# Kernel tuning notes

Measured on AMD Instinct MI355X. Metric: run time of the kernel, lower is better.

## Reference

```python
import jax, jax.numpy as jnp
import numpy as np

DIM, H, D, B, L = 1024, 8, 64, 1, 256


def silu(v):
    return v * jax.nn.sigmoid(v)


def setup_inputs() -> dict:
    key = jax.random.key(0)
    ks = jax.random.split(key, 12)
    n = lambda i, shape, scale=1.0: jax.random.normal(ks[i], shape, dtype=jnp.float32) * scale
    return {
        "x": n(0, (B, L, DIM)),
        "hidden_real": n(1, (B, H, D)),
        "hidden_imag": n(2, (B, H, D)),
        "w_in1": n(3, (DIM, DIM), 1.0 / np.sqrt(DIM)),
        "b_in1": jnp.zeros((DIM,), jnp.float32),
        "w_in2": n(4, (DIM, H * D * 4), 1.0 / np.sqrt(DIM)),
        "b_in2": jnp.zeros((H * D * 4,), jnp.float32),
        "w_out1": n(5, (H * D * 2, DIM), 1.0 / np.sqrt(H * D * 2)),
        "b_out1": jnp.zeros((DIM,), jnp.float32),
        "w_out2": n(6, (DIM, DIM), 1.0 / np.sqrt(DIM)),
        "b_out2": jnp.zeros((DIM,), jnp.float32),
        "mat_v_real": n(7, (H, D, D)),
        "mat_v_imag": n(8, (H, D, D)),
    }


def reference(x, hidden_real, hidden_imag, w_in1, b_in1, w_in2, b_in2,
              w_out1, b_out1, w_out2, b_out2, mat_v_real, mat_v_imag):
    batch, slen, _ = x.shape
    t = silu(x @ w_in1 + b_in1)
    t = t @ w_in2 + b_in2                       # (B, L, 4*H*D)
    z = t.reshape(batch, slen, H, D, 2, 2)      # [..., {x,a}, {re,im}]
    xc = jax.lax.complex(z[..., 0, 0], z[..., 0, 1])   # (B, L, H, D) complex
    ac = jax.lax.complex(z[..., 1, 0], z[..., 1, 1])

    # normalize a: unit phase * sigmoid(log(|a|^2)) magnitude
    mag2 = ac.real * ac.real + ac.imag * ac.imag
    ac = ac * (jax.lax.rsqrt(mag2) * jax.nn.sigmoid(jnp.log(mag2)))

    a_ln = jnp.log(ac)                          # (B, L, H, D) complex
    al = jnp.transpose(a_ln, (0, 2, 3, 1))      # (B, H, D, L)

    # triu-broadcast + cumsum along cols == the FFT conv-with-ones in the original
    idx = jnp.arange(slen)
    triu = idx[:, None] <= idx[None, :]          # row i, col j: keep j >= i
    tri = jnp.where(triu, al[..., None, :], 0.0)  # (B, H, D, L, L)
    cum = jnp.cumsum(tri, axis=-1)               # cum[i, k] = sum_{j=i..k} a_ln[j]
    keep = (idx[:, None] - 1) <= idx[None, :]    # triu(diagonal=-1)
    c = jnp.where(keep, jnp.exp(cum), 0.0)       # c[i,k] = prod_{j=i..k} a[j]; c[i,i-1]=1

    V = jax.lax.complex(mat_v_real, mat_v_imag)  # (H, D, D)
    Vinv = jnp.linalg.inv(V)
    hidden = jax.lax.complex(hidden_real, hidden_imag)  # (B, H, D)

    x_roll = jnp.concatenate([hidden.astype(xc.dtype)[:, None], xc[:, :-1]], axis=1)
    u = jnp.einsum('hno,blho->blhn', Vinv, x_roll)       # V^{-1} applied per head
    h = jnp.einsum('bholm,blho->bmho', c, u)             # banded product-scan
    h = h.at[:, -1].add(jnp.einsum('hno,bho->bhn', Vinv, xc[:, -1]))
    h = jnp.einsum('hno,blho->blhn', V, h)               # back to V-basis

    hidden_next = h[:, -1]                                # (B, H, D) complex
    hr = jnp.stack([h.real, h.imag], axis=-1).reshape(batch, slen, H * D * 2)
    y = silu(hr @ w_out1 + b_out1)
    y = y @ w_out2 + b_out2
    return y, hidden_next
```

## Files before the change

### kernel.cpp

```cpp
#include <hip/hip_runtime.h>
#include <math.h>

#define DIMN 1024
#define NH 8
#define ND 64
#define LSEQ 256
#define HD 512

typedef __attribute__((ext_vector_type(8))) short short8;
typedef __attribute__((ext_vector_type(4))) float f32x4;

__device__ __forceinline__ float2 cmul(float2 a, float2 b){
    return make_float2(a.x*b.x - a.y*b.y, a.x*b.y + a.y*b.x);
}
__device__ __forceinline__ ushort f2bf(float f){
    union { float f; unsigned u; } v; v.f = f;
    unsigned r = v.u + 0x7FFF + ((v.u >> 16) & 1);
    return (ushort)(r >> 16);
}

#define ISTR 65

__device__ __forceinline__ void inv_gj_blocked(const float* __restrict__ Vr,
        const float* __restrict__ Vi, float2* __restrict__ Vinv,
        int h, int tid, float2* Mx){
    for (int idx = tid; idx < 4096; idx += 512){
        int i = idx >> 6, j = idx & 63;
        Mx[i*ISTR + j] = make_float2(Vr[h*4096 + idx], Vi[h*4096 + idx]);
    }
    __syncthreads();
    const int w = tid >> 6, l = tid & 63;
    const int rbase = w*8;
    for (int kb = 0; kb < 8; ++kb){
        const int k0 = kb*8;
        if (w == 0){
            float2 pr[8];
            #pragma unroll
            for (int m = 0; m < 8; ++m) pr[m] = Mx[l*ISTR + k0 + m];
            #pragma unroll
            for (int k = 0; k < 8; ++k){
                const int gk = k0 + k;
                float2 d; d.x = __shfl(pr[k].x, gk); d.y = __shfl(pr[k].y, gk);
                float im = 1.f/(d.x*d.x + d.y*d.y);
                float2 p = make_float2(d.x*im, -d.y*im);
                float2 spr[8];
                #pragma unroll
                for (int m = 0; m < 8; ++m){
                    float2 t; t.x = __shfl(pr[m].x, gk); t.y = __shfl(pr[m].y, gk);
                    spr[m] = (m == k) ? p : cmul(t, p);
                }
                float2 f = pr[k];
                if (l == gk){
                    #pragma unroll
                    for (int m = 0; m < 8; ++m) pr[m] = spr[m];
                } else {
                    #pragma unroll
                    for (int m = 0; m < 8; ++m){
                        float2 u = cmul(f, spr[m]);
                        if (m == k){ pr[m].x = -u.x;  pr[m].y = -u.y;  }
                        else       { pr[m].x -= u.x;  pr[m].y -= u.y;  }
                    }
                }
            }
            #pragma unroll
            for (int m = 0; m < 8; ++m) Mx[l*ISTR + k0 + m] = pr[m];
        }
        __syncthreads();
        float2 br[8];
        #pragma unroll
        for (int m = 0; m < 8; ++m) br[m] = Mx[(k0+m)*ISTR + l];
        __syncthreads();
        if (((unsigned)(l - k0)) >= 8u){
            #pragma unroll
            for (int rr = 0; rr < 8; ++rr){
                const int r = rbase + rr;
                float2 acc;
                if (((unsigned)(r - k0)) < 8u){ acc.x = 0.f; acc.y = 0.f; }
                else acc = Mx[r*ISTR + l];
                #pragma unroll
                for (int m = 0; m < 8; ++m){
                    float2 Pv = Mx[r*ISTR + k0 + m];
                    acc.x += Pv.x*br[m].x - Pv.y*br[m].y;
                    acc.y += Pv.x*br[m].y + Pv.y*br[m].x;
                }
                Mx[r*ISTR + l] = acc;
            }
        }
        __syncthreads();
    }
    for (int idx = tid; idx < 4096; idx += 512){
        int i = idx >> 6, j = idx & 63;
        Vinv[h*4096 + idx] = Mx[i*ISTR + j];
    }
}

__device__ __forceinline__ void w3eff_tile(const float* __restrict__ Vr,
        const float* __restrict__ Vi, const float* __restrict__ w3,
        ushort* __restrict__ W3bt, int t, int tid, float* lds){
    const int n0 = (t & 31)*32;
    const int c0 = (t >> 5)*32;
    const int h  = c0 >> 7;
    const int og0 = (c0 & 127) >> 1;
    float* Vbr = lds;
    float* Vbi = lds + 1024;
    float* Wb  = lds + 2048;
    for (int q = tid; q < 1024; q += 512){
        int dd = q >> 4, oo = q & 15;
        Vbr[q] = Vr[(h*64+dd)*64 + og0 + oo];
        Vbi[q] = Vi[(h*64+dd)*64 + og0 + oo];
    }
    for (int q = tid; q < 4096; q += 512){
        int row = q >> 5, nn = q & 31;
        Wb[q] = w3[(h*128 + row)*1024 + n0 + nn];
    }
    __syncthreads();
    const int nn = tid & 31, oo = tid >> 5;
    float ar = 0.f, ai = 0.f;
    #pragma unroll 8
    for (int dd = 0; dd < 64; ++dd){
        float vr = Vbr[dd*16 + oo], vi = Vbi[dd*16 + oo];
        float w0 = Wb[(dd*2)*32 + nn], w1v = Wb[(dd*2+1)*32 + nn];
        ar += vr*w0 + vi*w1v;
        ai += -vi*w0 + vr*w1v;
    }
    W3bt[(n0+nn)*1024 + c0 + oo*2 + 0] = f2bf(ar);
    W3bt[(n0+nn)*1024 + c0 + oo*2 + 1] = f2bf(ai);
}

__global__ __launch_bounds__(512) void prep_kernel(
        const float* __restrict__ x,
        const float* __restrict__ w1, const float* __restrict__ w2,
        const float* __restrict__ w3, const float* __restrict__ w4,
        const float* __restrict__ Vr, const float* __restrict__ Vi,
        ushort* __restrict__ x_bf,
        ushort* __restrict__ w1t, ushort* __restrict__ w2t,
        ushort* __restrict__ W3bt, ushort* __restrict__ w4t,
        float2* __restrict__ Vinv){
    __shared__ float2 Mx[64*ISTR];
    const int b = blockIdx.x;
    const int tid = threadIdx.x;

    if (b < 8){
        inv_gj_blocked(Vr, Vi, Vinv, b, tid, Mx);
        return;
    }

    int widx = b - 8;
    if (widx < 128){
        int i = widx*512 + tid;
        float4 v = ((const float4*)x)[i];
        ushort4 u; u.x=f2bf(v.x); u.y=f2bf(v.y); u.z=f2bf(v.z); u.w=f2bf(v.w);
        ((ushort4*)x_bf)[i] = u;
        return;
    }
    widx -= 128;

    if (widx >= 2048){
        w3eff_tile(Vr, Vi, w3, W3bt, widx - 2048, tid, (float*)Mx);
        return;
    }

    const float* W; ushort* Wt; int K = 1024, N;
    if (widx < 512)            { W = w1; Wt = w1t; N = 1024; }
    else if (widx < 1536)      { W = w2; Wt = w2t; N = 2048; widx -= 512; }
    else                       { W = w4; Wt = w4t; N = 1024; widx -= 1536; }
    const int half = tid >> 8;
    const int t = widx*2 + half;
    const int tiles_n = N >> 5;
    const int n0 = (t % tiles_n) * 32, k0 = (t / tiles_n) * 32;
    float* tile = (float*)Mx + half*(32*33);
    const int tx = tid & 31, ty = (tid >> 5) & 7;
    #pragma unroll
    for (int i = 0; i < 4; ++i)
        tile[(ty + i*8)*33 + tx] = W[(k0 + ty + i*8)*N + n0 + tx];
    __syncthreads();
    #pragma unroll
    for (int i = 0; i < 4; ++i){
        int r = ty + i*8;
        Wt[(n0 + r)*K + k0 + tx] = f2bf(tile[tx*33 + r]);
    }
}

__global__ __launch_bounds__(512) void inv_kernel(const float* __restrict__ Vr,
                                                  const float* __restrict__ Vi,
                                                  float2* __restrict__ Vinv){
    __shared__ float2 Mx[64*ISTR];
    inv_gj_blocked(Vr, Vi, Vinv, blockIdx.x, threadIdx.x, Mx);
}

__global__ __launch_bounds__(256) void transpose_cvt(const float* __restrict__ W,
                 ushort* __restrict__ Wt, int K, int N){
    __shared__ float tile[32][33];
    const int n0 = blockIdx.x * 32, k0 = blockIdx.y * 32;
    const int tx = threadIdx.x & 31, ty = threadIdx.x >> 5;
    #pragma unroll
    for (int i = 0; i < 4; ++i)
        tile[ty + i*8][tx] = W[(k0 + ty + i*8)*N + n0 + tx];
    __syncthreads();
    #pragma unroll
    for (int i = 0; i < 4; ++i){
        int r = ty + i*8;
        Wt[(n0 + r)*K + k0 + tx] = f2bf(tile[tx][r]);
    }
}

__global__ __launch_bounds__(256) void cvt_bf16_kernel(const float* __restrict__ in,
                                 ushort* __restrict__ o, int n4){
    int i = blockIdx.x*256 + threadIdx.x;
    if (i < n4){
        float4 v = ((const float4*)in)[i];
        ushort4 u; u.x=f2bf(v.x); u.y=f2bf(v.y); u.z=f2bf(v.z); u.w=f2bf(v.w);
        ((ushort4*)o)[i] = u;
    }
}

#define BM 64
#define BN 64
#define BK 32
#define ASTR 40
template<int ACT>
__global__ __launch_bounds__(256) void gemm_bt(const ushort* __restrict__ A,
                 const ushort* __restrict__ Bt, const float* __restrict__ bias,
                 float* __restrict__ Cf, ushort* __restrict__ Cb,
                 float2* __restrict__ XCo, float2* __restrict__ Ao,
                 int M, int N, int K,
                 const float* __restrict__ tVr, const float* __restrict__ tVi,
                 const float2* __restrict__ S255, float* __restrict__ out_tail,
                 int tail_n){
    __shared__ ushort As[BM*ASTR];
    __shared__ ushort Bs[BN*ASTR];
    const int tid = threadIdx.x;
    const int bm = blockIdx.y * BM, bn = blockIdx.x * BN;
    const int wave = tid >> 6, l = tid & 63;
    const int wr = (wave >> 1) * 32, wc = (wave & 1) * 32;
    const int ml = l & 15, quad = l >> 4;

    if (ACT == 0 && out_tail != nullptr && blockIdx.x == 0 && blockIdx.y == 0){
        for (int hn = tid; hn < 512; hn += 256){
            int h = hn >> 6;
            float2 acc2 = make_float2(0.f, 0.f);
            #pragma unroll 8
            for (int o = 0; o < 64; ++o){
                float2 v = make_float2(tVr[hn*64+o], tVi[hn*64+o]);
                float2 p = cmul(v, S255[h*64+o]);
                acc2.x += p.x; acc2.y += p.y;
            }
            if (tail_n >= 1024){
                out_tail[hn]       = acc2.x;
                out_tail[512 + hn] = acc2.y;
            } else if (tail_n >= 512){
                out_tail[hn] = acc2.x;
            }
        }
    }

    f32x4 acc[2][2];
    #pragma unroll
    for (int i=0;i<2;++i)
        #pragma unroll
        for (int j=0;j<2;++j) acc[i][j] = (f32x4){0.f,0.f,0.f,0.f};
    const int c0r = tid >> 2;
    const int c0s = tid & 3;
    for (int k0 = 0; k0 < K; k0 += BK){
        uint4 av = *(const uint4*)&A [(bm + c0r)*K + k0 + c0s*8];
        uint4 bv = *(const uint4*)&Bt[(bn + c0r)*K + k0 + c0s*8];
        __syncthreads();
        *(uint4*)&As[c0r*ASTR + c0s*8] = av;
        *(uint4*)&Bs[c0r*ASTR + c0s*8] = bv;
        __syncthreads();
        short8 af[2], bfv[2];
        #pragma unroll
        for (int f=0; f<2; ++f){
            af[f]  = *(const short8*)&As[(wr + f*16 + ml)*ASTR + quad*8];
            bfv[f] = *(const short8*)&Bs[(wc + f*16 + ml)*ASTR + quad*8];
        }
        #pragma unroll
        for (int i=0;i<2;++i)
            #pragma unroll
            for (int j=0;j<2;++j)
                acc[i][j] = __builtin_amdgcn_mfma_f32_16x16x32_bf16(af[i], bfv[j], acc[i][j], 0,0,0);
    }
    #pragma unroll
    for (int i=0;i<2;++i){
        #pragma unroll
        for (int j=0;j<2;++j){
            const int gcol = bn + wc + j*16 + ml;
            const float bsv = bias[gcol];
            #pragma unroll
            for (int r=0;r<4;++r){
                const int grow = bm + wr + i*16 + quad*4 + r;
                float val = acc[i][j][r] + bsv;
                if (ACT == 2){
                    float v1 = __shfl_down(val, 1);
                    float v2 = __shfl_down(val, 2);
                    float v3 = __shfl_down(val, 3);
                    if ((l & 3) == 0){
                        int hd = gcol >> 2;
                        XCo[grow*HD + hd] = make_float2(val, v1);
                        float m2 = v2*v2 + v3*v3;
                        float s = sqrtf(m2)/(1.f + m2);
                        Ao[grow*HD + hd] = make_float2(v2*s, v3*s);
                    }
                } else if (ACT == 1){
                    val *= 1.f/(1.f + expf(-val));
                    Cb[grow*N + gcol] = f2bf(val);
                } else {
                    Cf[grow*N + gcol] = val;
                }
            }
        }
    }
}

__global__ __launch_bounds__(512) void upscan_kernel(const float2* __restrict__ Vinv,
        const float* __restrict__ hidr, const float* __restrict__ him,
        const float2* __restrict__ XC, const float2* __restrict__ Aseq,
        ushort* __restrict__ Sb, float2* __restrict__ S255){
    __shared__ float4 buf[2][2][LSEQ];
    __shared__ float2 vrow[2][64];
    __shared__ float2 inu[2];
    const int b = blockIdx.x;
    const int tid = threadIdx.x;
    const int g = tid >> 8, m = tid & 255;
    const int hn = b*2 + g;
    const int h = hn >> 6;
    if (m < 64) vrow[g][m] = Vinv[hn*64 + m];
    __syncthreads();
    float2 acc = make_float2(0.f, 0.f);
    const float2* xrow = &XC[m*HD + h*64];
    #pragma unroll 8
    for (int o=0;o<64;++o){
        float2 p = cmul(vrow[g][o], xrow[o]);
        acc.x += p.x; acc.y += p.y;
    }
    if (m == 0){
        float2 i0 = make_float2(0.f, 0.f);
        #pragma unroll 8
        for (int o=0;o<64;++o){
            float2 hv = make_float2(hidr[h*64+o], him[h*64+o]);
            float2 p = cmul(vrow[g][o], hv);
            i0.x += p.x; i0.y += p.y;
        }
        inu[g] = i0;
    }
    float2 a = Aseq[m*HD + hn];
    buf[0][g][m] = make_float4(a.x, a.y, acc.x, acc.y);
    __syncthreads();
    int pb = 0;
    #pragma unroll
    for (int d = 1; d < LSEQ; d <<= 1){
        float4 cur = buf[pb][g][m];
        float4 o2 = cur;
        if (m >= d){
            float4 prev = buf[pb][g][m-d];
            float2 cA = make_float2(cur.x, cur.y), cU = make_float2(cur.z, cur.w);
            float2 pA = make_float2(prev.x, prev.y), pU = make_float2(prev.z, prev.w);
            float2 nA = cmul(cA, pA);
            float2 nU = cmul(cA, pU);
            nU.x += cU.x; nU.y += cU.y;
            o2 = make_float4(nA.x, nA.y, nU.x, nU.y);
        }
        buf[pb^1][g][m] = o2;
        pb ^= 1;
        __syncthreads();
    }
    float4 t = buf[pb][g][m];
    float2 init = inu[g];
    float2 st = cmul(make_float2(t.x, t.y), init);
    st.x += t.z; st.y += t.w;
    Sb[m*DIMN + hn*2]   = f2bf(st.x);
    Sb[m*DIMN + hn*2+1] = f2bf(st.y);
    if (m == LSEQ-1) S255[hn] = st;
}

__global__ __launch_bounds__(256) void vmul_kernel(const float* __restrict__ Vr,
                            const float* __restrict__ Vi,
                            const float2* __restrict__ S, ushort* __restrict__ hrb,
                            float* __restrict__ out_tail, int tail_n){
    int g = blockIdx.x*256 + threadIdx.x;
    int m = g >> 9, hn = g & 511;
    int h = hn >> 6;
    const float* vr = &Vr[hn*64];
    const float* vi = &Vi[hn*64];
    const float2* srow = &S[m*HD + h*64];
    float2 acc = make_float2(0.f, 0.f);
    #pragma unroll 8
    for (int o=0;o<64;++o){
        float2 v = make_float2(vr[o], vi[o]);
        float2 p = cmul(v, srow[o]);
        acc.x += p.x; acc.y += p.y;
    }
    hrb[m*DIMN + hn*2]   = f2bf(acc.x);
    hrb[m*DIMN + hn*2+1] = f2bf(acc.y);
    if (m == LSEQ-1){
        if (tail_n >= 1024){
            out_tail[hn]       = acc.x;
            out_tail[512 + hn] = acc.y;
        } else if (tail_n >= 512){
            out_tail[hn] = acc.x;
        }
    }
}

__global__ __launch_bounds__(512) void upscan_f32_kernel(const float2* __restrict__ Vinv,
        const float* __restrict__ hidr, const float* __restrict__ him,
        const float2* __restrict__ XC, const float2* __restrict__ Aseq,
        float2* __restrict__ S){
    __shared__ float4 buf[2][2][LSEQ];
    __shared__ float2 vrow[2][64];
    __shared__ float2 inu[2];
    const int b = blockIdx.x;
    const int tid = threadIdx.x;
    const int g = tid >> 8, m = tid & 255;
    const int hn = b*2 + g;
    const int h = hn >> 6;
    if (m < 64) vrow[g][m] = Vinv[hn*64 + m];
    __syncthreads();
    float2 acc = make_float2(0.f, 0.f);
    const float2* xrow = &XC[m*HD + h*64];
    #pragma unroll 8
    for (int o=0;o<64;++o){
        float2 p = cmul(vrow[g][o], xrow[o]);
        acc.x += p.x; acc.y += p.y;
    }
    if (m == 0){
        float2 i0 = make_float2(0.f, 0.f);
        #pragma unroll 8
        for (int o=0;o<64;++o){
            float2 hv = make_float2(hidr[h*64+o], him[h*64+o]);
            float2 p = cmul(vrow[g][o], hv);
            i0.x += p.x; i0.y += p.y;
        }
        inu[g] = i0;
    }
    float2 a = Aseq[m*HD + hn];
    buf[0][g][m] = make_float4(a.x, a.y, acc.x, acc.y);
    __syncthreads();
    int pb = 0;
    #pragma unroll
    for (int d = 1; d < LSEQ; d <<= 1){
        float4 cur = buf[pb][g][m];
        float4 o2 = cur;
        if (m >= d){
            float4 prev = buf[pb][g][m-d];
            float2 cA = make_float2(cur.x, cur.y), cU = make_float2(cur.z, cur.w);
            float2 pA = make_float2(prev.x, prev.y), pU = make_float2(prev.z, prev.w);
            float2 nA = cmul(cA, pA);
            float2 nU = cmul(cA, pU);
            nU.x += cU.x; nU.y += cU.y;
            o2 = make_float4(nA.x, nA.y, nU.x, nU.y);
        }
        buf[pb^1][g][m] = o2;
        pb ^= 1;
        __syncthreads();
    }
    float4 t = buf[pb][g][m];
    float2 init = inu[g];
    float2 st = cmul(make_float2(t.x, t.y), init);
    st.x += t.z; st.y += t.w;
    S[m*HD + hn] = st;
}

extern "C" void kernel_launch(void* const* d_in, const int* in_sizes, int n_in,
                              void* d_out, int out_size, void* d_ws, size_t ws_size,
                              hipStream_t stream) {
    const float* x      = (const float*)d_in[0];
    const float* hidr   = (const float*)d_in[1];
    const float* hidi   = (const float*)d_in[2];
    const float* w_in1  = (const float*)d_in[3];
    const float* b_in1  = (const float*)d_in[4];
    const float* w_in2  = (const float*)d_in[5];
    const float* b_in2  = (const float*)d_in[6];
    const float* w_out1 = (const float*)d_in[7];
    const float* b_out1 = (const float*)d_in[8];
    const float* w_out2 = (const float*)d_in[9];
    const float* b_out2 = (const float*)d_in[10];
    const float* Vr     = (const float*)d_in[11];
    const float* Vi     = (const float*)d_in[12];
    float* out = (float*)d_out;
    const int tail_n = out_size - LSEQ*DIMN;
    char* ws = (char*)d_ws;

    if (ws_size >= 14946304u){
        float2* Vinv  = (float2*)(ws + 0);
        ushort* w1t   = (ushort*)(ws + 262144);
        ushort* w2t   = (ushort*)(ws + 2359296);
        ushort* W3bt  = (ushort*)(ws + 6553600);
        ushort* w4t   = (ushort*)(ws + 8650752);
        ushort* x_bf  = (ushort*)(ws + 10747904);
        ushort* t1_bf = (ushort*)(ws + 11272192);
        float2* XC    = (float2*)(ws + 11796480);
        float2* Aseq  = (float2*)(ws + 12845056);
        float2* S255  = (float2*)(ws + 13893632);
        ushort* y1_bf = x_bf;
        ushort* Sb    = t1_bf;

        prep_kernel<<<3208, 512, 0, stream>>>(x, w_in1, w_in2, w_out1, w_out2,
                                              Vr, Vi, x_bf, w1t, w2t, W3bt, w4t, Vinv);
        gemm_bt<1><<<dim3(16,4), 256, 0, stream>>>(x_bf, w1t, b_in1, nullptr, t1_bf,
                nullptr, nullptr, LSEQ, DIMN, DIMN, nullptr, nullptr, nullptr, nullptr, 0);
        gemm_bt<2><<<dim3(32,4), 256, 0, stream>>>(t1_bf, w2t, b_in2, nullptr, nullptr,
                XC, Aseq, LSEQ, 2048, DIMN, nullptr, nullptr, nullptr, nullptr, 0);
        upscan_kernel<<<256, 512, 0, stream>>>(Vinv, hidr, hidi, XC, Aseq, Sb, S255);
        gemm_bt<1><<<dim3(16,4), 256, 0, stream>>>(Sb, W3bt, b_out1, nullptr, y1_bf,
                nullptr, nullptr, LSEQ, DIMN, DIMN, nullptr, nullptr, nullptr, nullptr, 0);
        gemm_bt<0><<<dim3(16,4), 256, 0, stream>>>(y1_bf, w4t, b_out2, out, nullptr,
                nullptr, nullptr, LSEQ, DIMN, DIMN, Vr, Vi, S255, out + LSEQ*DIMN, tail_n);
    } else {
        float2* Vinv  = (float2*)(ws + 0);
        ushort* wt    = (ushort*)(ws + 262144);
        ushort* x_bf  = (ushort*)(ws + 4456448);
        ushort* t1_bf = (ushort*)(ws + 4980736);
        float2* XC    = (float2*)(ws + 5505024);
        float2* Aseq  = (float2*)(ws + 6553600);
        float2* S     = (float2*)(ws + 7602176);
        ushort* y1_bf = x_bf;
        ushort* hr_bf = t1_bf;

        inv_kernel<<<NH, 512, 0, stream>>>(Vr, Vi, Vinv);
        cvt_bf16_kernel<<<LSEQ*DIMN/4/256, 256, 0, stream>>>(x, x_bf, LSEQ*DIMN/4);
        transpose_cvt<<<dim3(32,32), 256, 0, stream>>>(w_in1, wt, DIMN, DIMN);
        gemm_bt<1><<<dim3(16,4), 256, 0, stream>>>(x_bf, wt, b_in1, nullptr, t1_bf,
                nullptr, nullptr, LSEQ, DIMN, DIMN, nullptr, nullptr, nullptr, nullptr, 0);
        transpose_cvt<<<dim3(64,32), 256, 0, stream>>>(w_in2, wt, DIMN, 2048);
        gemm_bt<2><<<dim3(32,4), 256, 0, stream>>>(t1_bf, wt, b_in2, nullptr, nullptr,
                XC, Aseq, LSEQ, 2048, DIMN, nullptr, nullptr, nullptr, nullptr, 0);
        upscan_f32_kernel<<<256, 512, 0, stream>>>(Vinv, hidr, hidi, XC, Aseq, S);
        vmul_kernel<<<LSEQ*HD/256, 256, 0, stream>>>(Vr, Vi, S, hr_bf, out + LSEQ*DIMN, tail_n);
        transpose_cvt<<<dim3(32,32), 256, 0, stream>>>(w_out1, wt, DIMN, DIMN);
        gemm_bt<1><<<dim3(16,4), 256, 0, stream>>>(hr_bf, wt, b_out1, nullptr, y1_bf,
                nullptr, nullptr, LSEQ, DIMN, DIMN, nullptr, nullptr, nullptr, nullptr, 0);
        transpose_cvt<<<dim3(32,32), 256, 0, stream>>>(w_out2, wt, DIMN, DIMN);
        gemm_bt<0><<<dim3(16,4), 256, 0, stream>>>(y1_bf, wt, b_out2, out, nullptr,
                nullptr, nullptr, LSEQ, DIMN, DIMN, nullptr, nullptr, nullptr, nullptr, 0);
    }
}
```

Before: 212.7 us.

## Fuse first GEMM into prep kernel reading fp32 x and w1 directly

The first GEMM (x @ w_in1 + bias, SiLU) now runs inside the prep kernel as 32 extra blocks, each computing two 64x64 tiles. These tiles load fp32 x and w1 directly and convert to bf16 in LDS. This removes the separate x conversion, the w1 transpose/convert pass and one kernel launch. The cost is that the GEMM runs alongside the other prep work with no software pipelining, and it does strided scalar loads of w1 that may be poorly coalesced.

```diff
diff --git a/kernel.cpp b/kernel.cpp
--- a/kernel.cpp
+++ b/kernel.cpp
@@ -20,6 +20,8 @@
 }
 
 #define ISTR 65
+#define ASTR 40
+#define BK 32
 
 __device__ __forceinline__ void inv_gj_blocked(const float* __restrict__ Vr,
         const float* __restrict__ Vi, float2* __restrict__ Vinv,
@@ -127,48 +129,102 @@
     W3bt[(n0+nn)*1024 + c0 + oo*2 + 1] = f2bf(ai);
 }
 
-__global__ __launch_bounds__(512) void prep_kernel(
+__device__ __forceinline__ void gemm1_direct_tile(const float* __restrict__ x,
+        const float* __restrict__ w1, const float* __restrict__ bias,
+        ushort* __restrict__ Cb, int tile, int tid8, ushort* lds){
+    ushort* As = lds;
+    ushort* Bs = lds + 64*ASTR;
+    const int bm = (tile & 3)*64, bn = (tile >> 2)*64;
+    const int wave = tid8 >> 6, l = tid8 & 63;
+    const int wr = (wave >> 1)*32, wc = (wave & 1)*32;
+    const int ml = l & 15, quad = l >> 4;
+    f32x4 acc[2][2];
+    #pragma unroll
+    for (int i=0;i<2;++i)
+        #pragma unroll
+        for (int j=0;j<2;++j) acc[i][j] = (f32x4){0.f,0.f,0.f,0.f};
+    const int c0r = tid8 >> 2, c0s = tid8 & 3;
+    const int bn_n = tid8 & 63, bk0 = (tid8 >> 6)*8;
+    for (int k0 = 0; k0 < DIMN; k0 += BK){
+        float4 a0 = *(const float4*)&x[(bm+c0r)*DIMN + k0 + c0s*8];
+        float4 a1 = *(const float4*)&x[(bm+c0r)*DIMN + k0 + c0s*8 + 4];
+        float bv[8];
+        #pragma unroll
+        for (int kk = 0; kk < 8; ++kk)
+            bv[kk] = w1[(k0 + bk0 + kk)*DIMN + bn + bn_n];
+        __syncthreads();
+        ushort4 u0; u0.x=f2bf(a0.x); u0.y=f2bf(a0.y); u0.z=f2bf(a0.z); u0.w=f2bf(a0.w);
+        ushort4 u1; u1.x=f2bf(a1.x); u1.y=f2bf(a1.y); u1.z=f2bf(a1.z); u1.w=f2bf(a1.w);
+        *(ushort4*)&As[c0r*ASTR + c0s*8]     = u0;
+        *(ushort4*)&As[c0r*ASTR + c0s*8 + 4] = u1;
+        #pragma unroll
+        for (int kk = 0; kk < 8; ++kk)
+            Bs[bn_n*ASTR + bk0 + kk] = f2bf(bv[kk]);
+        __syncthreads();
+        short8 af[2], bfv[2];
+        #pragma unroll
+        for (int f=0; f<2; ++f){
+            af[f]  = *(const short8*)&As[(wr + f*16 + ml)*ASTR + quad*8];
+            bfv[f] = *(const short8*)&Bs[(wc + f*16 + ml)*ASTR + quad*8];
+        }
+        #pragma unroll
+        for (int i=0;i<2;++i)
+            #pragma unroll
+            for (int j=0;j<2;++j)
+                acc[i][j] = __builtin_amdgcn_mfma_f32_16x16x32_bf16(af[i], bfv[j], acc[i][j], 0,0,0);
+    }
+    #pragma unroll
+    for (int i=0;i<2;++i){
+        #pragma unroll
+        for (int j=0;j<2;++j){
+            const int gcol = bn + wc + j*16 + ml;
+            const float bsv = bias[gcol];
+            #pragma unroll
+            for (int r=0;r<4;++r){
+                const int grow = bm + wr + i*16 + quad*4 + r;
+                float val = acc[i][j][r] + bsv;
+                val *= 1.f/(1.f + expf(-val));
+                Cb[grow*DIMN + gcol] = f2bf(val);
+            }
+        }
+    }
+}
+
+__global__ __launch_bounds__(512) void mix1_kernel(
         const float* __restrict__ x,
         const float* __restrict__ w1, const float* __restrict__ w2,
         const float* __restrict__ w3, const float* __restrict__ w4,
         const float* __restrict__ Vr, const float* __restrict__ Vi,
-        ushort* __restrict__ x_bf,
-        ushort* __restrict__ w1t, ushort* __restrict__ w2t,
-        ushort* __restrict__ W3bt, ushort* __restrict__ w4t,
-        float2* __restrict__ Vinv){
-    __shared__ float2 Mx[64*ISTR];
+        const float* __restrict__ b1,
+        ushort* __restrict__ t1_bf,
+        ushort* __restrict__ w2t, ushort* __restrict__ W3bt,
+        ushort* __restrict__ w4t, float2* __restrict__ Vinv){
+    __shared__ __align__(16) char lds_raw[33280];
     const int b = blockIdx.x;
     const int tid = threadIdx.x;
-
-    if (b < 8){
-        inv_gj_blocked(Vr, Vi, Vinv, b, tid, Mx);
+    const int half = tid >> 8;
+
+    if (b < 32){
+        gemm1_direct_tile(x, w1, b1, t1_bf, b*2 + half, tid & 255,
+                          (ushort*)lds_raw + half*(128*ASTR));
         return;
     }
-
-    int widx = b - 8;
-    if (widx < 128){
-        int i = widx*512 + tid;
-        float4 v = ((const float4*)x)[i];
-        ushort4 u; u.x=f2bf(v.x); u.y=f2bf(v.y); u.z=f2bf(v.z); u.w=f2bf(v.w);
-        ((ushort4*)x_bf)[i] = u;
+    if (b < 40){
+        inv_gj_blocked(Vr, Vi, Vinv, b - 32, tid, (float2*)lds_raw);
         return;
     }
-    widx -= 128;
-
-    if (widx >= 2048){
-        w3eff_tile(Vr, Vi, w3, W3bt, widx - 2048, tid, (float*)Mx);
+    int widx = b - 40;
+    if (widx >= 1536){
+        w3eff_tile(Vr, Vi, w3, W3bt, widx - 1536, tid, (float*)lds_raw);
         return;
     }
-
     const float* W; ushort* Wt; int K = 1024, N;
-    if (widx < 512)            { W = w1; Wt = w1t; N = 1024; }
-    else if (widx < 1536)      { W = w2; Wt = w2t; N = 2048; widx -= 512; }
-    else                       { W = w4; Wt = w4t; N = 1024; widx -= 1536; }
-    const int half = tid >> 8;
+    if (widx < 1024){ W = w2; Wt = w2t; N = 2048; }
+    else            { W = w4; Wt = w4t; N = 1024; widx -= 1024; }
     const int t = widx*2 + half;
     const int tiles_n = N >> 5;
     const int n0 = (t % tiles_n) * 32, k0 = (t / tiles_n) * 32;
-    float* tile = (float*)Mx + half*(32*33);
+    float* tile = (float*)lds_raw + half*(32*33);
     const int tx = tid & 31, ty = (tid >> 5) & 7;
     #pragma unroll
     for (int i = 0; i < 4; ++i)
@@ -216,8 +272,6 @@
 
 #define BM 64
 #define BN 64
-#define BK 32
-#define ASTR 40
 template<int ACT>
 __global__ __launch_bounds__(256) void gemm_bt(const ushort* __restrict__ A,
                  const ushort* __restrict__ Bt, const float* __restrict__ bias,
@@ -483,22 +537,18 @@
 
     if (ws_size >= 14946304u){
         float2* Vinv  = (float2*)(ws + 0);
-        ushort* w1t   = (ushort*)(ws + 262144);
         ushort* w2t   = (ushort*)(ws + 2359296);
         ushort* W3bt  = (ushort*)(ws + 6553600);
         ushort* w4t   = (ushort*)(ws + 8650752);
-        ushort* x_bf  = (ushort*)(ws + 10747904);
+        ushort* y1_bf = (ushort*)(ws + 10747904);
         ushort* t1_bf = (ushort*)(ws + 11272192);
         float2* XC    = (float2*)(ws + 11796480);
         float2* Aseq  = (float2*)(ws + 12845056);
         float2* S255  = (float2*)(ws + 13893632);
-        ushort* y1_bf = x_bf;
         ushort* Sb    = t1_bf;
 
-        prep_kernel<<<3208, 512, 0, stream>>>(x, w_in1, w_in2, w_out1, w_out2,
-                                              Vr, Vi, x_bf, w1t, w2t, W3bt, w4t, Vinv);
-        gemm_bt<1><<<dim3(16,4), 256, 0, stream>>>(x_bf, w1t, b_in1, nullptr, t1_bf,
-                nullptr, nullptr, LSEQ, DIMN, DIMN, nullptr, nullptr, nullptr, nullptr, 0);
+        mix1_kernel<<<2600, 512, 0, stream>>>(x, w_in1, w_in2, w_out1, w_out2,
+                                              Vr, Vi, b_in1, t1_bf, w2t, W3bt, w4t, Vinv);
         gemm_bt<2><<<dim3(32,4), 256, 0, stream>>>(t1_bf, w2t, b_in2, nullptr, nullptr,
                 XC, Aseq, LSEQ, 2048, DIMN, nullptr, nullptr, nullptr, nullptr, 0);
         upscan_kernel<<<256, 512, 0, stream>>>(Vinv, hidr, hidi, XC, Aseq, Sb, S255);
```

New measurement: 198.0 us. 1.07x faster.
